# Kernel optimization log

Hardware: AMD Instinct MI355X
Metric: run time of the kernel (lower is better)

Reference implementation:

```python
import jax, jax.numpy as jnp
import numpy as np

GAMMA = 0.95
T, B = 256, 1024


def setup_inputs() -> dict:
    key = jax.random.key(0)
    ks = jax.random.split(key, 6)
    return {
        "state_trajectory_action_values": jax.random.normal(ks[0], (T, B), jnp.float32),
        "target_state_trajectory_action_values": jax.random.normal(ks[1], (T, B), jnp.float32),
        "target_state_current_action_values": jax.random.normal(ks[2], (T, B), jnp.float32),
        "rewards": jax.random.normal(ks[3], (T, B), jnp.float32),
        # small-scale log-probs so cumulative clamped importance weights stay in exp range
        "original_log_trajectory_action_probs": jax.random.normal(ks[4], (T, B), jnp.float32) * 0.01,
        "target_log_trajectory_task_action_probs": jax.random.normal(ks[5], (T, B), jnp.float32) * 0.01,
    }


def reference(state_trajectory_action_values,
              target_state_trajectory_action_values,
              target_state_current_action_values,
              rewards,
              original_log_trajectory_action_probs,
              target_log_trajectory_task_action_probs):
    num_steps = state_trajectory_action_values.shape[0]
    # clamp(min=0) as in the torch module
    lw = jnp.clip(target_log_trajectory_task_action_probs
                  - original_log_trajectory_action_probs, 0.0, None)  # [T, B]
    # exclusive prefix sum: P[t] = sum_{k < t} lw[k]
    P = jnp.cumsum(lw, axis=0) - lw  # [T, B]
    idx = jnp.arange(num_steps)
    log_gamma = jnp.log(jnp.asarray(GAMMA, lw.dtype))
    # logW[i, j] = (j - i) * log(gamma) + P[j] - P[i]  ==  log(gamma^(j-i) * exp(sum lw[i:j]))
    logW = (idx[None, :] - idx[:, None]).astype(lw.dtype) * log_gamma  # [T, T]
    logW = logW[:, :, None] + (P[None, :, :] - P[:, None, :])          # [T, T, B]
    mask = (idx[None, :] >= idx[:, None])[:, :, None]                  # j >= i
    W = jnp.where(mask, jnp.exp(logW), 0.0)                            # [T, T, B]
    # retrace[i] = sum_{j>=i} W[i,j] * (r[j] + tq_curr[i] - tq_traj[j])
    A = rewards - target_state_trajectory_action_values               # [T, B]
    retrace = (jnp.einsum('ijb,jb->ib', W, A)
               + target_state_current_action_values * W.sum(axis=1))  # [T, B]
    diff = state_trajectory_action_values - retrace
    return jnp.mean(diff * diff)
```

## Files before the change

kernel.cpp:

```cpp
#include <hip/hip_runtime.h>


constexpr int   T     = 256;
constexpr int   B     = 1024;
constexpr float GAMMA = 0.95f;

constexpr int CPB  = 16;
constexpr int NBLK = B / CPB;
constexpr int RPT  = 4;
constexpr int NSEG = T / RPT;

__global__ __launch_bounds__(NSEG * CPB) void retrace_main(
    const float* __restrict__ q,
    const float* __restrict__ tq_traj,
    const float* __restrict__ tq_curr,
    const float* __restrict__ rewards,
    const float* __restrict__ olp,
    const float* __restrict__ tlp,
    float* __restrict__ partials)
{
    const int col  = threadIdx.x & (CPB - 1);
    const int seg  = threadIdx.x >> 4;
    const int gcol = blockIdx.x * CPB + col;
    const int r0   = seg * RPT;

    float cb[RPT], Ab[RPT], qb[RPT], tb[RPT];
    float R = 0.f, W = 0.f, C = 1.f;
    #pragma unroll
    for (int k = RPT - 1; k >= 0; --k) {
        const int idx = (r0 + k) * B + gcol;
        const float lw = fmaxf(tlp[idx] - olp[idx], 0.f);
        const float c  = GAMMA * __expf(lw);
        const float A  = rewards[idx] - tq_traj[idx];
        cb[k] = c;  Ab[k] = A;
        qb[k] = q[idx];  tb[k] = tq_curr[idx];
        R = fmaf(c, R, A);
        W = fmaf(c, W, 1.f);
        C *= c;
    }

    __shared__ float sR[2][NSEG][CPB + 1];
    __shared__ float sW[2][NSEG][CPB + 1];
    __shared__ float sC[2][NSEG][CPB + 1];

    int p = 0;
    sR[0][seg][col] = R;
    sW[0][seg][col] = W;
    sC[0][seg][col] = C;
    __syncthreads();

    #pragma unroll
    for (int d = 1; d < NSEG; d <<= 1) {
        float r = sR[p][seg][col];
        float w = sW[p][seg][col];
        float c = sC[p][seg][col];
        if (seg + d < NSEG) {
            r = fmaf(c, sR[p][seg + d][col], r);
            w = fmaf(c, sW[p][seg + d][col], w);
            c = c * sC[p][seg + d][col];
        }
        sR[p ^ 1][seg][col] = r;
        sW[p ^ 1][seg][col] = w;
        sC[p ^ 1][seg][col] = c;
        __syncthreads();
        p ^= 1;
    }

    float Rc = 0.f, Wc = 0.f;
    if (seg + 1 < NSEG) {
        Rc = sR[p][seg + 1][col];
        Wc = sW[p][seg + 1][col];
    }

    float acc = 0.f;
    #pragma unroll
    for (int k = RPT - 1; k >= 0; --k) {
        Rc = fmaf(cb[k], Rc, Ab[k]);
        Wc = fmaf(cb[k], Wc, 1.f);
        const float retrace = fmaf(tb[k], Wc, Rc);
        const float d = qb[k] - retrace;
        acc = fmaf(d, d, acc);
    }

    #pragma unroll
    for (int off = 32; off > 0; off >>= 1)
        acc += __shfl_down(acc, off, 64);

    __shared__ float sw[16];
    const int lane = threadIdx.x & 63, wv = threadIdx.x >> 6;
    if (lane == 0) sw[wv] = acc;
    __syncthreads();
    if (threadIdx.x == 0) {
        float t = 0.f;
        #pragma unroll
        for (int i = 0; i < 16; ++i) t += sw[i];
        partials[blockIdx.x] = t;
    }
}

__global__ void retrace_final(const float* __restrict__ partials,
                              float* __restrict__ out)
{
    float v = (threadIdx.x < NBLK) ? partials[threadIdx.x] : 0.f;
    #pragma unroll
    for (int off = 32; off > 0; off >>= 1)
        v += __shfl_down(v, off, 64);
    if (threadIdx.x == 0) out[0] = v / (float)(T * B);
}

extern "C" void kernel_launch(void* const* d_in, const int* in_sizes, int n_in,
                              void* d_out, int out_size, void* d_ws, size_t ws_size,
                              hipStream_t stream)
{
    const float* q       = (const float*)d_in[0];
    const float* tq_traj = (const float*)d_in[1];
    const float* tq_curr = (const float*)d_in[2];
    const float* rewards = (const float*)d_in[3];
    const float* olp     = (const float*)d_in[4];
    const float* tlp     = (const float*)d_in[5];

    float* partials = (float*)d_ws;
    float* out      = (float*)d_out;

    retrace_main<<<NBLK, NSEG * CPB, 0, stream>>>(
        q, tq_traj, tq_curr, rewards, olp, tlp, partials);
    retrace_final<<<1, 64, 0, stream>>>(partials, out);
}
```

Baseline: 10.95 us.

## Scan one row per thread over narrower column tiles with swizzled block order

Removes the per-thread serial 4-row segment, so every thread holds one timestep and the Hillis-Steele scan runs over all 256 rows. Blocks now cover 4 columns instead of 16, which gives 256 blocks, and the block index is swizzled into a column tile. The final reduction grows to 256 partials using a two-level shuffle plus shared-memory sum. This adds more parallelism and blocks, but the scan now needs 8 synchronized steps instead of 6, and global accesses are only 16 bytes contiguous per row.

```diff
diff --git a/kernel.cpp b/kernel.cpp
--- a/kernel.cpp
+++ b/kernel.cpp
@@ -5,10 +5,9 @@
 constexpr int   B     = 1024;
 constexpr float GAMMA = 0.95f;
 
-constexpr int CPB  = 16;
+constexpr int CPB  = 4;
 constexpr int NBLK = B / CPB;
-constexpr int RPT  = 4;
-constexpr int NSEG = T / RPT;
+constexpr int NSEG = T;
 
 __global__ __launch_bounds__(NSEG * CPB) void retrace_main(
     const float* __restrict__ q,
@@ -19,68 +18,51 @@
     const float* __restrict__ tlp,
     float* __restrict__ partials)
 {
-    const int col  = threadIdx.x & (CPB - 1);
-    const int seg  = threadIdx.x >> 4;
-    const int gcol = blockIdx.x * CPB + col;
-    const int r0   = seg * RPT;
+    const int col = threadIdx.x & (CPB - 1);
+    const int seg = threadIdx.x >> 2;
+    const int bi   = blockIdx.x;
+    const int tile = ((bi & 7) << 5) | (bi >> 3);
+    const int gcol = tile * CPB + col;
+    const int idx  = seg * B + gcol;
 
-    float cb[RPT], Ab[RPT], qb[RPT], tb[RPT];
-    float R = 0.f, W = 0.f, C = 1.f;
-    #pragma unroll
-    for (int k = RPT - 1; k >= 0; --k) {
-        const int idx = (r0 + k) * B + gcol;
-        const float lw = fmaxf(tlp[idx] - olp[idx], 0.f);
-        const float c  = GAMMA * __expf(lw);
-        const float A  = rewards[idx] - tq_traj[idx];
-        cb[k] = c;  Ab[k] = A;
-        qb[k] = q[idx];  tb[k] = tq_curr[idx];
-        R = fmaf(c, R, A);
-        W = fmaf(c, W, 1.f);
-        C *= c;
-    }
+    const float lw = fmaxf(tlp[idx] - olp[idx], 0.f);
+    const float c  = GAMMA * __expf(lw);
+    const float A  = rewards[idx] - tq_traj[idx];
+    const float qv = q[idx];
+    const float tc = tq_curr[idx];
 
     __shared__ float sR[2][NSEG][CPB + 1];
     __shared__ float sW[2][NSEG][CPB + 1];
     __shared__ float sC[2][NSEG][CPB + 1];
 
     int p = 0;
-    sR[0][seg][col] = R;
-    sW[0][seg][col] = W;
-    sC[0][seg][col] = C;
+    sR[0][seg][col] = A;
+    sW[0][seg][col] = 1.f;
+    sC[0][seg][col] = c;
     __syncthreads();
 
     #pragma unroll
     for (int d = 1; d < NSEG; d <<= 1) {
         float r = sR[p][seg][col];
         float w = sW[p][seg][col];
-        float c = sC[p][seg][col];
+        float cc = sC[p][seg][col];
         if (seg + d < NSEG) {
-            r = fmaf(c, sR[p][seg + d][col], r);
-            w = fmaf(c, sW[p][seg + d][col], w);
-            c = c * sC[p][seg + d][col];
+            r  = fmaf(cc, sR[p][seg + d][col], r);
+            w  = fmaf(cc, sW[p][seg + d][col], w);
+            cc = cc * sC[p][seg + d][col];
         }
         sR[p ^ 1][seg][col] = r;
         sW[p ^ 1][seg][col] = w;
-        sC[p ^ 1][seg][col] = c;
+        sC[p ^ 1][seg][col] = cc;
         __syncthreads();
         p ^= 1;
     }
 
-    float Rc = 0.f, Wc = 0.f;
-    if (seg + 1 < NSEG) {
-        Rc = sR[p][seg + 1][col];
-        Wc = sW[p][seg + 1][col];
-    }
-
-    float acc = 0.f;
-    #pragma unroll
-    for (int k = RPT - 1; k >= 0; --k) {
-        Rc = fmaf(cb[k], Rc, Ab[k]);
-        Wc = fmaf(cb[k], Wc, 1.f);
-        const float retrace = fmaf(tb[k], Wc, Rc);
-        const float d = qb[k] - retrace;
-        acc = fmaf(d, d, acc);
-    }
+    const float R = sR[p][seg][col];
+    const float W = sW[p][seg][col];
+    const float retrace = fmaf(tc, W, R);
+    const float d0 = qv - retrace;
+    float acc = d0 * d0;
 
     #pragma unroll
     for (int off = 32; off > 0; off >>= 1)
@@ -94,18 +76,25 @@
         float t = 0.f;
         #pragma unroll
         for (int i = 0; i < 16; ++i) t += sw[i];
-        partials[blockIdx.x] = t;
+        partials[bi] = t;
     }
 }
 
-__global__ void retrace_final(const float* __restrict__ partials,
-                              float* __restrict__ out)
+__global__ __launch_bounds__(256) void retrace_final(
+    const float* __restrict__ partials,
+    float* __restrict__ out)
 {
-    float v = (threadIdx.x < NBLK) ? partials[threadIdx.x] : 0.f;
+    float v = partials[threadIdx.x];
     #pragma unroll
     for (int off = 32; off > 0; off >>= 1)
         v += __shfl_down(v, off, 64);
-    if (threadIdx.x == 0) out[0] = v / (float)(T * B);
+
+    __shared__ float sw[4];
+    const int lane = threadIdx.x & 63, wv = threadIdx.x >> 6;
+    if (lane == 0) sw[wv] = v;
+    __syncthreads();
+    if (threadIdx.x == 0)
+        out[0] = (sw[0] + sw[1] + sw[2] + sw[3]) / (float)(T * B);
 }
 
 extern "C" void kernel_launch(void* const* d_in, const int* in_sizes, int n_in,
@@ -124,5 +113,5 @@
 
     retrace_main<<<NBLK, NSEG * CPB, 0, stream>>>(
         q, tq_traj, tq_curr, rewards, olp, tlp, partials);
-    retrace_final<<<1, 64, 0, stream>>>(partials, out);
+    retrace_final<<<1, 256, 0, stream>>>(partials, out);
 }
```

Measured after the change: 12.15 us. 11.0% more time.
